# Kernel tuning notes

Measured on AMD Instinct MI355X. Metric: run time of the kernel, lower is better.

## Reference

```python
import jax, jax.numpy as jnp
import numpy as np

MB, SEQ, EMBDIM, N_TOKENS = 8, 2048, 64, 8192


def setup_inputs() -> dict:
    key = jax.random.key(0)
    k1, k2 = jax.random.split(key)
    X = jax.random.normal(k1, (MB, SEQ, EMBDIM), dtype=jnp.float32)
    weight = jax.random.normal(k2, (N_TOKENS, EMBDIM), dtype=jnp.float32)
    return {"X": X, "weight": weight}


def reference(X, weight):
    adotb = jnp.einsum("bse,ne->bsn", X, weight)            # [mb, seq, n_tokens]
    adota = jnp.sum(X * X, axis=-1, keepdims=True)           # [mb, seq, 1]
    bdotb = jnp.sum(weight * weight, axis=-1)                # [n_tokens]
    dist = adota - 2.0 * adotb + bdotb                       # [mb, seq, n_tokens]
    return jnp.argmin(dist, axis=-1)                         # [mb, seq] int indices
```

## Files before the change

kernel.cpp:

```cpp
#include <hip/hip_runtime.h>
#include <math.h>

#define EMB     64
#define NTOK    8192
#define NQ      16384
#define TPB     256
#define CSPLIT  4
#define CRANGE  (NTOK / CSPLIT)
#define BQ      128
#define TILE_C  128
#define NT      (CRANGE / TILE_C)
#define TCH     (TILE_C * EMB)

typedef _Float16 half8 __attribute__((ext_vector_type(8)));
typedef float    f32x4 __attribute__((ext_vector_type(4)));

__device__ __forceinline__ void gl2lds16(const _Float16* g, _Float16* l) {
    __builtin_amdgcn_global_load_lds(
        (const __attribute__((address_space(1))) unsigned int*)g,
        (__attribute__((address_space(3))) unsigned int*)l, 16, 0, 0);
}

__global__ void ynorm_kernel(const float* __restrict__ W, float* __restrict__ ynorm) {
    int c = blockIdx.x * blockDim.x + threadIdx.x;
    if (c >= NTOK) return;
    const float4* w4 = (const float4*)(W + (size_t)c * EMB);
    float s = 0.f;
#pragma unroll
    for (int i = 0; i < EMB / 4; ++i) {
        float4 v = w4[i];
        s = fmaf(v.x, v.x, s); s = fmaf(v.y, v.y, s);
        s = fmaf(v.z, v.z, s); s = fmaf(v.w, v.w, s);
    }
    ynorm[c] = s;
}

__global__ void wsplit_kernel(const float* __restrict__ W,
                              _Float16* __restrict__ Wh, _Float16* __restrict__ Wl) {
    int u = blockIdx.x * blockDim.x + threadIdx.x;
    int g    = u >> 7;
    int rem  = u & 127;
    int kb   = rem >> 6;
    int lane = rem & 63;
    int r    = lane & 15, lq = lane >> 4;
    int c    = g * 16 + r;
    int k0   = kb * 32 + lq * 8;
    const float* wp = W + (size_t)c * EMB + k0;
    float4 v0 = *(const float4*)wp;
    float4 v1 = *(const float4*)(wp + 4);
    float xv[8] = {v0.x, v0.y, v0.z, v0.w, v1.x, v1.y, v1.z, v1.w};
    half8 h, l;
#pragma unroll
    for (int j = 0; j < 8; ++j) {
        _Float16 hh = (_Float16)xv[j];
        h[j] = hh;
        l[j] = (_Float16)(xv[j] - (float)hh);
    }
    *(half8*)(Wh + (size_t)u * 8) = h;
    *(half8*)(Wl + (size_t)u * 8) = l;
}

__global__ __launch_bounds__(TPB, 2) void vq_mfma_kernel(
    const float* __restrict__ X,
    const _Float16* __restrict__ Wh, const _Float16* __restrict__ Wl,
    const float* __restrict__ ynorm,
    float* __restrict__ pval, int* __restrict__ pidx)
{
    __shared__ __align__(16) _Float16 LdsH0[TCH];
    __shared__ __align__(16) _Float16 LdsH1[TCH];
    __shared__ __align__(16) _Float16 LdsL0[TCH];
    __shared__ __align__(16) _Float16 LdsL1[TCH];
    __shared__ __align__(16) float    Lyn[CRANGE];
    __shared__ float RedV[2][BQ];
    __shared__ int   RedI[2][BQ];

    const int t    = threadIdx.x;
    const int lane = t & 63;
    const int wid  = t >> 6;
    const int wq   = wid & 1;
    const int wy   = wid >> 1;
    const int l15  = lane & 15;
    const int lq   = lane >> 4;

    const int qblk   = blockIdx.x * BQ;
    const int qbase  = qblk + wq * 64;
    const int cbase0 = blockIdx.y * CRANGE;

    {
        const size_t gsbase = (size_t)(cbase0 >> 4) * 1024;
#pragma unroll
        for (int i = 0; i < 4; ++i) {
            const int jw = i * 256 + wid * 64;
            gl2lds16(Wh + gsbase + (size_t)(jw + lane) * 8, LdsH0 + (size_t)jw * 8);
            gl2lds16(Wl + gsbase + (size_t)(jw + lane) * 8, LdsL0 + (size_t)jw * 8);
        }
    }

    for (int u = t; u < CRANGE / 4; u += TPB)
        ((float4*)Lyn)[u] = ((const float4*)(ynorm + cbase0))[u];

    half8 ah[4][2], al[4][2];
#pragma unroll
    for (int mt = 0; mt < 4; ++mt) {
#pragma unroll
        for (int kb = 0; kb < 2; ++kb) {
            const float* xp = X + (size_t)(qbase + mt * 16 + l15) * EMB + kb * 32 + lq * 8;
            float4 v0 = *(const float4*)xp;
            float4 v1 = *(const float4*)(xp + 4);
            float xv[8] = {v0.x, v0.y, v0.z, v0.w, v1.x, v1.y, v1.z, v1.w};
            half8 h, l;
#pragma unroll
            for (int j = 0; j < 8; ++j) {
                _Float16 hh = (_Float16)xv[j];
                h[j] = hh;
                l[j] = (_Float16)(xv[j] - (float)hh);
            }
            ah[mt][kb] = h;
            al[mt][kb] = l;
        }
    }

    float minv[4][4];
    int   mini[4][4];
#pragma unroll
    for (int mt = 0; mt < 4; ++mt)
#pragma unroll
        for (int r = 0; r < 4; ++r) { minv[mt][r] = INFINITY; mini[mt][r] = 0; }

    const f32x4 zero4 = {0.f, 0.f, 0.f, 0.f};

    __syncthreads();

    int cur = 0;
    for (int tt = 0; tt < NT; ++tt) {
        if (tt + 1 < NT) {
            const size_t gsbase = (size_t)((cbase0 + (tt + 1) * TILE_C) >> 4) * 1024;
            _Float16* dH = (cur ^ 1) ? LdsH1 : LdsH0;
            _Float16* dL = (cur ^ 1) ? LdsL1 : LdsL0;
#pragma unroll
            for (int i = 0; i < 4; ++i) {
                const int jw = i * 256 + wid * 64;
                gl2lds16(Wh + gsbase + (size_t)(jw + lane) * 8, dH + (size_t)jw * 8);
                gl2lds16(Wl + gsbase + (size_t)(jw + lane) * 8, dL + (size_t)jw * 8);
            }
        }

        const _Float16* LH = cur ? LdsH1 : LdsH0;
        const _Float16* LL = cur ? LdsL1 : LdsL0;
        const int c0 = tt * TILE_C;
#pragma unroll
        for (int ct = 0; ct < 4; ++ct) {
            const int chunk0 = (wy * 4 + ct) * 128 + lane;
            half8 bh0 = *(const half8*)(LH + (size_t)chunk0 * 8);
            half8 bl0 = *(const half8*)(LL + (size_t)chunk0 * 8);
            half8 bh1 = *(const half8*)(LH + (size_t)(chunk0 + 64) * 8);
            half8 bl1 = *(const half8*)(LL + (size_t)(chunk0 + 64) * 8);
            f32x4 acc[4];
#pragma unroll
            for (int mt = 0; mt < 4; ++mt) {
                f32x4 a = __builtin_amdgcn_mfma_f32_16x16x32_f16(al[mt][0], bl0, zero4, 0, 0, 0);
                a = __builtin_amdgcn_mfma_f32_16x16x32_f16(al[mt][0], bh0, a, 0, 0, 0);
                a = __builtin_amdgcn_mfma_f32_16x16x32_f16(ah[mt][0], bl0, a, 0, 0, 0);
                a = __builtin_amdgcn_mfma_f32_16x16x32_f16(ah[mt][0], bh0, a, 0, 0, 0);
                a = __builtin_amdgcn_mfma_f32_16x16x32_f16(al[mt][1], bl1, a, 0, 0, 0);
                a = __builtin_amdgcn_mfma_f32_16x16x32_f16(al[mt][1], bh1, a, 0, 0, 0);
                a = __builtin_amdgcn_mfma_f32_16x16x32_f16(ah[mt][1], bl1, a, 0, 0, 0);
                a = __builtin_amdgcn_mfma_f32_16x16x32_f16(ah[mt][1], bh1, a, 0, 0, 0);
                acc[mt] = a;
            }
            const int   ccol = wy * 64 + ct * 16;
            const float yn   = Lyn[c0 + ccol + l15];
            const int   cidx = cbase0 + c0 + ccol + l15;
#pragma unroll
            for (int mt = 0; mt < 4; ++mt) {
#pragma unroll
                for (int r = 0; r < 4; ++r) {
                    float s = fmaf(-2.f, acc[mt][r], yn);
                    if (s < minv[mt][r]) { minv[mt][r] = s; mini[mt][r] = cidx; }
                }
            }
        }

        asm volatile("s_waitcnt vmcnt(0)" ::: "memory");
        asm volatile("s_waitcnt lgkmcnt(0)" ::: "memory");
        __builtin_amdgcn_s_barrier();
        cur ^= 1;
    }

#pragma unroll
    for (int mt = 0; mt < 4; ++mt) {
#pragma unroll
        for (int r = 0; r < 4; ++r) {
            float v = minv[mt][r];
            int   i = mini[mt][r];
#pragma unroll
            for (int m = 1; m <= 8; m <<= 1) {
                float ov = __shfl_xor(v, m, 64);
                int   oi = __shfl_xor(i, m, 64);
                if (ov < v || (ov == v && oi < i)) { v = ov; i = oi; }
            }
            if (l15 == 0) {
                int qoff = wq * 64 + mt * 16 + lq * 4 + r;
                RedV[wy][qoff] = v;
                RedI[wy][qoff] = i;
            }
        }
    }
    __syncthreads();

    if (t < BQ) {
        float v0 = RedV[0][t]; int i0 = RedI[0][t];
        float v1 = RedV[1][t]; int i1 = RedI[1][t];
        if (v1 < v0 || (v1 == v0 && i1 < i0)) { v0 = v1; i0 = i1; }
        size_t o = (size_t)blockIdx.y * NQ + qblk + t;
        pval[o] = v0;
        pidx[o] = i0;
    }
}

__global__ void combine_kernel(const float* __restrict__ pval,
                               const int* __restrict__ pidx,
                               int* __restrict__ out)
{
    int q = blockIdx.x * blockDim.x + threadIdx.x;
    if (q >= NQ) return;
    float bv = pval[q];
    int   bi = pidx[q];
#pragma unroll
    for (int s = 1; s < CSPLIT; ++s) {
        float v  = pval[(size_t)s * NQ + q];
        int   i2 = pidx[(size_t)s * NQ + q];
        if (v < bv || (v == bv && i2 < bi)) { bv = v; bi = i2; }
    }
    out[q] = bi;
}

extern "C" void kernel_launch(void* const* d_in, const int* in_sizes, int n_in,
                              void* d_out, int out_size, void* d_ws, size_t ws_size,
                              hipStream_t stream) {
    const float* X = (const float*)d_in[0];
    const float* W = (const float*)d_in[1];

    _Float16* Wh    = (_Float16*)d_ws;
    _Float16* Wl    = Wh + (size_t)NTOK * EMB;
    float*    ynorm = (float*)(Wl + (size_t)NTOK * EMB);
    float*    pval  = ynorm + NTOK;
    int*      pidx  = (int*)(pval + (size_t)CSPLIT * NQ);
    int*      out   = (int*)d_out;

    ynorm_kernel<<<NTOK / TPB, TPB, 0, stream>>>(W, ynorm);
    wsplit_kernel<<<(NTOK * 8) / TPB, TPB, 0, stream>>>(W, Wh, Wl);
    dim3 grid(NQ / BQ, CSPLIT);
    vq_mfma_kernel<<<grid, TPB, 0, stream>>>(X, Wh, Wl, ynorm, pval, pidx);
    combine_kernel<<<NQ / TPB, TPB, 0, stream>>>(pval, pidx, out);
}
```

Baseline: 126.7 us.

## Fuse weight prep kernels and enlarge query blocks with wider codebook split

```diff
diff --git a/kernel.cpp b/kernel.cpp
--- a/kernel.cpp
+++ b/kernel.cpp
@@ -4,12 +4,9 @@
 #define EMB     64
 #define NTOK    8192
 #define NQ      16384
-#define TPB     256
-#define CSPLIT  4
-#define CRANGE  (NTOK / CSPLIT)
-#define BQ      128
+#define TPB     512
+#define BQ      256
 #define TILE_C  128
-#define NT      (CRANGE / TILE_C)
 #define TCH     (TILE_C * EMB)
 
 typedef _Float16 half8 __attribute__((ext_vector_type(8)));
@@ -21,51 +18,45 @@
         (__attribute__((address_space(3))) unsigned int*)l, 16, 0, 0);
 }
 
-__global__ void ynorm_kernel(const float* __restrict__ W, float* __restrict__ ynorm) {
+__global__ void prep_kernel(const float* __restrict__ W,
+                            _Float16* __restrict__ Wh, _Float16* __restrict__ Wl,
+                            float* __restrict__ ynorm) {
     int c = blockIdx.x * blockDim.x + threadIdx.x;
     if (c >= NTOK) return;
-    const float4* w4 = (const float4*)(W + (size_t)c * EMB);
+    const int g = c >> 4, r = c & 15;
+    const float* wp = W + (size_t)c * EMB;
     float s = 0.f;
 #pragma unroll
-    for (int i = 0; i < EMB / 4; ++i) {
-        float4 v = w4[i];
-        s = fmaf(v.x, v.x, s); s = fmaf(v.y, v.y, s);
-        s = fmaf(v.z, v.z, s); s = fmaf(v.w, v.w, s);
+    for (int seg = 0; seg < 8; ++seg) {
+        float4 v0 = *(const float4*)(wp + seg * 8);
+        float4 v1 = *(const float4*)(wp + seg * 8 + 4);
+        float xv[8] = {v0.x, v0.y, v0.z, v0.w, v1.x, v1.y, v1.z, v1.w};
+        half8 h, l;
+#pragma unroll
+        for (int j = 0; j < 8; ++j) {
+            _Float16 hh = (_Float16)xv[j];
+            h[j] = hh;
+            l[j] = (_Float16)(xv[j] - (float)hh);
+            s = fmaf(xv[j], xv[j], s);
+        }
+        const int kb = seg >> 2, lq = seg & 3;
+        const size_t u = (size_t)g * 128 + kb * 64 + lq * 16 + r;
+        *(half8*)(Wh + u * 8) = h;
+        *(half8*)(Wl + u * 8) = l;
     }
     ynorm[c] = s;
 }
 
-__global__ void wsplit_kernel(const float* __restrict__ W,
-                              _Float16* __restrict__ Wh, _Float16* __restrict__ Wl) {
-    int u = blockIdx.x * blockDim.x + threadIdx.x;
-    int g    = u >> 7;
-    int rem  = u & 127;
-    int kb   = rem >> 6;
-    int lane = rem & 63;
-    int r    = lane & 15, lq = lane >> 4;
-    int c    = g * 16 + r;
-    int k0   = kb * 32 + lq * 8;
-    const float* wp = W + (size_t)c * EMB + k0;
-    float4 v0 = *(const float4*)wp;
-    float4 v1 = *(const float4*)(wp + 4);
-    float xv[8] = {v0.x, v0.y, v0.z, v0.w, v1.x, v1.y, v1.z, v1.w};
-    half8 h, l;
-#pragma unroll
-    for (int j = 0; j < 8; ++j) {
-        _Float16 hh = (_Float16)xv[j];
-        h[j] = hh;
-        l[j] = (_Float16)(xv[j] - (float)hh);
-    }
-    *(half8*)(Wh + (size_t)u * 8) = h;
-    *(half8*)(Wl + (size_t)u * 8) = l;
-}
-
-__global__ __launch_bounds__(TPB, 2) void vq_mfma_kernel(
+template <int CS>
+__global__ __launch_bounds__(TPB, 4) void vq_mfma_kernel(
     const float* __restrict__ X,
     const _Float16* __restrict__ Wh, const _Float16* __restrict__ Wl,
     const float* __restrict__ ynorm,
     float* __restrict__ pval, int* __restrict__ pidx)
 {
+    constexpr int CRANGE = NTOK / CS;
+    constexpr int NT     = CRANGE / TILE_C;
+
     __shared__ __align__(16) _Float16 LdsH0[TCH];
     __shared__ __align__(16) _Float16 LdsH1[TCH];
     __shared__ __align__(16) _Float16 LdsL0[TCH];
@@ -77,8 +68,8 @@
     const int t    = threadIdx.x;
     const int lane = t & 63;
     const int wid  = t >> 6;
-    const int wq   = wid & 1;
-    const int wy   = wid >> 1;
+    const int wq   = wid & 3;
+    const int wy   = wid >> 2;
     const int l15  = lane & 15;
     const int lq   = lane >> 4;
 
@@ -89,8 +80,8 @@
     {
         const size_t gsbase = (size_t)(cbase0 >> 4) * 1024;
 #pragma unroll
-        for (int i = 0; i < 4; ++i) {
-            const int jw = i * 256 + wid * 64;
+        for (int i = 0; i < 2; ++i) {
+            const int jw = i * 512 + wid * 64;
             gl2lds16(Wh + gsbase + (size_t)(jw + lane) * 8, LdsH0 + (size_t)jw * 8);
             gl2lds16(Wl + gsbase + (size_t)(jw + lane) * 8, LdsL0 + (size_t)jw * 8);
         }
@@ -138,8 +129,8 @@
             _Float16* dH = (cur ^ 1) ? LdsH1 : LdsH0;
             _Float16* dL = (cur ^ 1) ? LdsL1 : LdsL0;
 #pragma unroll
-            for (int i = 0; i < 4; ++i) {
-                const int jw = i * 256 + wid * 64;
+            for (int i = 0; i < 2; ++i) {
+                const int jw = i * 512 + wid * 64;
                 gl2lds16(Wh + gsbase + (size_t)(jw + lane) * 8, dH + (size_t)jw * 8);
                 gl2lds16(Wl + gsbase + (size_t)(jw + lane) * 8, dL + (size_t)jw * 8);
             }
@@ -218,6 +209,7 @@
     }
 }
 
+template <int CS>
 __global__ void combine_kernel(const float* __restrict__ pval,
                                const int* __restrict__ pidx,
                                int* __restrict__ out)
@@ -227,7 +219,7 @@
     float bv = pval[q];
     int   bi = pidx[q];
 #pragma unroll
-    for (int s = 1; s < CSPLIT; ++s) {
+    for (int s = 1; s < CS; ++s) {
         float v  = pval[(size_t)s * NQ + q];
         int   i2 = pidx[(size_t)s * NQ + q];
         if (v < bv || (v == bv && i2 < bi)) { bv = v; bi = i2; }
@@ -245,12 +237,20 @@
     _Float16* Wl    = Wh + (size_t)NTOK * EMB;
     float*    ynorm = (float*)(Wl + (size_t)NTOK * EMB);
     float*    pval  = ynorm + NTOK;
-    int*      pidx  = (int*)(pval + (size_t)CSPLIT * NQ);
     int*      out   = (int*)d_out;
 
-    ynorm_kernel<<<NTOK / TPB, TPB, 0, stream>>>(W, ynorm);
-    wsplit_kernel<<<(NTOK * 8) / TPB, TPB, 0, stream>>>(W, Wh, Wl);
-    dim3 grid(NQ / BQ, CSPLIT);
-    vq_mfma_kernel<<<grid, TPB, 0, stream>>>(X, Wh, Wl, ynorm, pval, pidx);
-    combine_kernel<<<NQ / TPB, TPB, 0, stream>>>(pval, pidx, out);
-}
+    prep_kernel<<<NTOK / 256, 256, 0, stream>>>(W, Wh, Wl, ynorm);
+
+    const size_t fixed = 2u * NTOK * EMB * sizeof(_Float16) + NTOK * sizeof(float);
+    if (ws_size >= fixed + (size_t)8 * NQ * 8) {
+        int* pidx = (int*)(pval + (size_t)8 * NQ);
+        dim3 grid(NQ / BQ, 8);
+        vq_mfma_kernel<8><<<grid, TPB, 0, stream>>>(X, Wh, Wl, ynorm, pval, pidx);
+        combine_kernel<8><<<NQ / 256, 256, 0, stream>>>(pval, pidx, out);
+    } else {
+        int* pidx = (int*)(pval + (size_t)4 * NQ);
+        dim3 grid(NQ / BQ, 4);
+        vq_mfma_kernel<4><<<grid, TPB, 0, stream>>>(X, Wh, Wl, ynorm, pval, pidx);
+        combine_kernel<4><<<NQ / 256, 256, 0, stream>>>(pval, pidx, out);
+    }
+}
```

Result: slower. 296.0 us (+133.5%).

## Fuse prep, main and combine into one cooperative kernel with grid syncs

Applied to the files above, without the earlier changes.

```diff
diff --git a/kernel.cpp b/kernel.cpp
--- a/kernel.cpp
+++ b/kernel.cpp
@@ -1,5 +1,8 @@
 #include <hip/hip_runtime.h>
+#include <hip/hip_cooperative_groups.h>
 #include <math.h>
+
+namespace cg = cooperative_groups;
 
 #define EMB     64
 #define NTOK    8192
@@ -7,10 +10,12 @@
 #define TPB     256
 #define CSPLIT  4
 #define CRANGE  (NTOK / CSPLIT)
+#define NT      (CRANGE / 128)
 #define BQ      128
 #define TILE_C  128
-#define NT      (CRANGE / TILE_C)
 #define TCH     (TILE_C * EMB)
+#define NXBLK   (NQ / BQ)
+#define NGRID   (NXBLK * CSPLIT)
 
 typedef _Float16 half8 __attribute__((ext_vector_type(8)));
 typedef float    f32x4 __attribute__((ext_vector_type(4)));
@@ -21,46 +26,47 @@
         (__attribute__((address_space(3))) unsigned int*)l, 16, 0, 0);
 }
 
-__global__ void ynorm_kernel(const float* __restrict__ W, float* __restrict__ ynorm) {
-    int c = blockIdx.x * blockDim.x + threadIdx.x;
-    if (c >= NTOK) return;
-    const float4* w4 = (const float4*)(W + (size_t)c * EMB);
-    float s = 0.f;
-#pragma unroll
-    for (int i = 0; i < EMB / 4; ++i) {
-        float4 v = w4[i];
-        s = fmaf(v.x, v.x, s); s = fmaf(v.y, v.y, s);
-        s = fmaf(v.z, v.z, s); s = fmaf(v.w, v.w, s);
-    }
-    ynorm[c] = s;
-}
-
-__global__ void wsplit_kernel(const float* __restrict__ W,
-                              _Float16* __restrict__ Wh, _Float16* __restrict__ Wl) {
-    int u = blockIdx.x * blockDim.x + threadIdx.x;
-    int g    = u >> 7;
-    int rem  = u & 127;
-    int kb   = rem >> 6;
-    int lane = rem & 63;
-    int r    = lane & 15, lq = lane >> 4;
-    int c    = g * 16 + r;
-    int k0   = kb * 32 + lq * 8;
-    const float* wp = W + (size_t)c * EMB + k0;
-    float4 v0 = *(const float4*)wp;
-    float4 v1 = *(const float4*)(wp + 4);
-    float xv[8] = {v0.x, v0.y, v0.z, v0.w, v1.x, v1.y, v1.z, v1.w};
-    half8 h, l;
-#pragma unroll
-    for (int j = 0; j < 8; ++j) {
-        _Float16 hh = (_Float16)xv[j];
-        h[j] = hh;
-        l[j] = (_Float16)(xv[j] - (float)hh);
-    }
-    *(half8*)(Wh + (size_t)u * 8) = h;
-    *(half8*)(Wl + (size_t)u * 8) = l;
-}
-
-__global__ __launch_bounds__(TPB, 2) void vq_mfma_kernel(
+__device__ __forceinline__ void vq_prep_phase(
+    int gtid, const float* __restrict__ W,
+    _Float16* __restrict__ Wh, _Float16* __restrict__ Wl,
+    float* __restrict__ ynorm)
+{
+    if (gtid < NTOK * 8) {
+        const int u = gtid;
+        const int g = u >> 7, rem = u & 127;
+        const int kb = rem >> 6, ln = rem & 63;
+        const int r = ln & 15, lq2 = ln >> 4;
+        const int c = g * 16 + r;
+        const int k0 = kb * 32 + lq2 * 8;
+        const float* wp = W + (size_t)c * EMB + k0;
+        float4 v0 = *(const float4*)wp;
+        float4 v1 = *(const float4*)(wp + 4);
+        float xv[8] = {v0.x, v0.y, v0.z, v0.w, v1.x, v1.y, v1.z, v1.w};
+        half8 h, l;
+#pragma unroll
+        for (int j = 0; j < 8; ++j) {
+            _Float16 hh = (_Float16)xv[j];
+            h[j] = hh;
+            l[j] = (_Float16)(xv[j] - (float)hh);
+        }
+        *(half8*)(Wh + (size_t)u * 8) = h;
+        *(half8*)(Wl + (size_t)u * 8) = l;
+    } else if (gtid < NTOK * 8 + NTOK) {
+        const int c = gtid - NTOK * 8;
+        const float4* w4 = (const float4*)(W + (size_t)c * EMB);
+        float s = 0.f;
+#pragma unroll
+        for (int i = 0; i < EMB / 4; ++i) {
+            float4 v = w4[i];
+            s = fmaf(v.x, v.x, s); s = fmaf(v.y, v.y, s);
+            s = fmaf(v.z, v.z, s); s = fmaf(v.w, v.w, s);
+        }
+        ynorm[c] = s;
+    }
+}
+
+__device__ __forceinline__ void vq_main_phase(
+    int bx, int by,
     const float* __restrict__ X,
     const _Float16* __restrict__ Wh, const _Float16* __restrict__ Wl,
     const float* __restrict__ ynorm,
@@ -82,9 +88,9 @@
     const int l15  = lane & 15;
     const int lq   = lane >> 4;
 
-    const int qblk   = blockIdx.x * BQ;
+    const int qblk   = bx * BQ;
     const int qbase  = qblk + wq * 64;
-    const int cbase0 = blockIdx.y * CRANGE;
+    const int cbase0 = by * CRANGE;
 
     {
         const size_t gsbase = (size_t)(cbase0 >> 4) * 1024;
@@ -148,14 +154,17 @@
         const _Float16* LH = cur ? LdsH1 : LdsH0;
         const _Float16* LL = cur ? LdsL1 : LdsL0;
         const int c0 = tt * TILE_C;
+
+        int chunk0 = (wy * 4) * 128 + lane;
+        half8 bh0 = *(const half8*)(LH + (size_t)chunk0 * 8);
+        half8 bl0 = *(const half8*)(LL + (size_t)chunk0 * 8);
+        half8 bh1 = *(const half8*)(LH + (size_t)(chunk0 + 64) * 8);
+        half8 bl1 = *(const half8*)(LL + (size_t)(chunk0 + 64) * 8);
+
 #pragma unroll
         for (int ct = 0; ct < 4; ++ct) {
-            const int chunk0 = (wy * 4 + ct) * 128 + lane;
-            half8 bh0 = *(const half8*)(LH + (size_t)chunk0 * 8);
-            half8 bl0 = *(const half8*)(LL + (size_t)chunk0 * 8);
-            half8 bh1 = *(const half8*)(LH + (size_t)(chunk0 + 64) * 8);
-            half8 bl1 = *(const half8*)(LL + (size_t)(chunk0 + 64) * 8);
             f32x4 acc[4];
+            __builtin_amdgcn_s_setprio(1);
 #pragma unroll
             for (int mt = 0; mt < 4; ++mt) {
                 f32x4 a = __builtin_amdgcn_mfma_f32_16x16x32_f16(al[mt][0], bl0, zero4, 0, 0, 0);
@@ -168,6 +177,16 @@
                 a = __builtin_amdgcn_mfma_f32_16x16x32_f16(ah[mt][1], bh1, a, 0, 0, 0);
                 acc[mt] = a;
             }
+            __builtin_amdgcn_s_setprio(0);
+
+            if (ct < 3) {
+                const int cn = (wy * 4 + ct + 1) * 128 + lane;
+                bh0 = *(const half8*)(LH + (size_t)cn * 8);
+                bl0 = *(const half8*)(LL + (size_t)cn * 8);
+                bh1 = *(const half8*)(LH + (size_t)(cn + 64) * 8);
+                bl1 = *(const half8*)(LL + (size_t)(cn + 64) * 8);
+            }
+
             const int   ccol = wy * 64 + ct * 16;
             const float yn   = Lyn[c0 + ccol + l15];
             const int   cidx = cbase0 + c0 + ccol + l15;
@@ -212,17 +231,16 @@
         float v0 = RedV[0][t]; int i0 = RedI[0][t];
         float v1 = RedV[1][t]; int i1 = RedI[1][t];
         if (v1 < v0 || (v1 == v0 && i1 < i0)) { v0 = v1; i0 = i1; }
-        size_t o = (size_t)blockIdx.y * NQ + qblk + t;
+        size_t o = (size_t)by * NQ + qblk + t;
         pval[o] = v0;
         pidx[o] = i0;
     }
 }
 
-__global__ void combine_kernel(const float* __restrict__ pval,
-                               const int* __restrict__ pidx,
-                               int* __restrict__ out)
+__device__ __forceinline__ void vq_combine_phase(
+    int q, const float* __restrict__ pval, const int* __restrict__ pidx,
+    int* __restrict__ out)
 {
-    int q = blockIdx.x * blockDim.x + threadIdx.x;
     if (q >= NQ) return;
     float bv = pval[q];
     int   bi = pidx[q];
@@ -233,6 +251,45 @@
         if (v < bv || (v == bv && i2 < bi)) { bv = v; bi = i2; }
     }
     out[q] = bi;
+}
+
+__global__ __launch_bounds__(TPB, 2) void vq_coop_kernel(
+    const float* __restrict__ X, const float* __restrict__ W,
+    _Float16* __restrict__ Wh, _Float16* __restrict__ Wl,
+    float* __restrict__ ynorm,
+    float* __restrict__ pval, int* __restrict__ pidx, int* __restrict__ out)
+{
+    cg::grid_group grid = cg::this_grid();
+    const int gtid = blockIdx.x * TPB + threadIdx.x;
+
+    vq_prep_phase(gtid, W, Wh, Wl, ynorm);
+    __threadfence();
+    grid.sync();
+
+    vq_main_phase(blockIdx.x & (NXBLK - 1), blockIdx.x >> 7,
+                  X, Wh, Wl, ynorm, pval, pidx);
+    __threadfence();
+    grid.sync();
+
+    vq_combine_phase(gtid, pval, pidx, out);
+}
+
+__global__ void prep_kernel_f(const float* __restrict__ W,
+                              _Float16* __restrict__ Wh, _Float16* __restrict__ Wl,
+                              float* __restrict__ ynorm) {
+    vq_prep_phase(blockIdx.x * 256 + threadIdx.x, W, Wh, Wl, ynorm);
+}
+__global__ __launch_bounds__(TPB, 2) void vq_main_kernel_f(
+    const float* __restrict__ X,
+    const _Float16* __restrict__ Wh, const _Float16* __restrict__ Wl,
+    const float* __restrict__ ynorm,
+    float* __restrict__ pval, int* __restrict__ pidx) {
+    vq_main_phase(blockIdx.x, blockIdx.y, X, Wh, Wl, ynorm, pval, pidx);
+}
+__global__ void combine_kernel_f(const float* __restrict__ pval,
+                                 const int* __restrict__ pidx,
+                                 int* __restrict__ out) {
+    vq_combine_phase(blockIdx.x * 256 + threadIdx.x, pval, pidx, out);
 }
 
 extern "C" void kernel_launch(void* const* d_in, const int* in_sizes, int n_in,
@@ -248,9 +305,16 @@
     int*      pidx  = (int*)(pval + (size_t)CSPLIT * NQ);
     int*      out   = (int*)d_out;
 
-    ynorm_kernel<<<NTOK / TPB, TPB, 0, stream>>>(W, ynorm);
-    wsplit_kernel<<<(NTOK * 8) / TPB, TPB, 0, stream>>>(W, Wh, Wl);
-    dim3 grid(NQ / BQ, CSPLIT);
-    vq_mfma_kernel<<<grid, TPB, 0, stream>>>(X, Wh, Wl, ynorm, pval, pidx);
-    combine_kernel<<<NQ / TPB, TPB, 0, stream>>>(pval, pidx, out);
-}
+    void* args[] = {(void*)&X, (void*)&W, (void*)&Wh, (void*)&Wl,
+                    (void*)&ynorm, (void*)&pval, (void*)&pidx, (void*)&out};
+    hipError_t e = hipLaunchCooperativeKernel((const void*)vq_coop_kernel,
+                                              dim3(NGRID), dim3(TPB),
+                                              args, 0, stream);
+    if (e != hipSuccess) {
+        (void)hipGetLastError();
+        prep_kernel_f<<<(NTOK * 8 + NTOK) / 256, 256, 0, stream>>>(W, Wh, Wl, ynorm);
+        dim3 grid(NXBLK, CSPLIT);
+        vq_main_kernel_f<<<grid, TPB, 0, stream>>>(X, Wh, Wl, ynorm, pval, pidx);
+        combine_kernel_f<<<NQ / 256, 256, 0, stream>>>(pval, pidx, out);
+    }
+}
```

Measured after the change: 298.3 us. 2.35x slower.
